# Kernel optimization log

Measured on AMD Instinct MI355X. Metric: run time of the kernel, lower is better.

The kernel has to match this reference:

```python
import math
import jax, jax.numpy as jnp
import numpy as np

B, S, T = 32, 512, 180
D, F, L, H = 512, 2048, 6, 8
DH = D // H


def _pos_encoding(length, d):
    pos = np.arange(length, dtype=np.float32)[:, None]
    div = np.exp(np.arange(0, d, 2, dtype=np.float32) * (-math.log(10000.0) / d))
    pe = np.zeros((length, d), dtype=np.float32)
    pe[:, 0::2] = np.sin(pos * div)
    pe[:, 1::2] = np.cos(pos * div)
    return jnp.asarray(pe)


def _ln(x, scale, bias):
    mu = x.mean(-1, keepdims=True)
    var = ((x - mu) ** 2).mean(-1, keepdims=True)
    return (x - mu) * jax.lax.rsqrt(var + 1e-5) * scale + bias


def _mha(q_in, kv_in, w, b, causal=False):
    # w: [4, D, D] = (Wq, Wk, Wv, Wo); b: [4, D]
    b_, sq = q_in.shape[:2]
    q = (q_in @ w[0] + b[0]).reshape(b_, sq, H, DH)
    k = (kv_in @ w[1] + b[1]).reshape(b_, -1, H, DH)
    v = (kv_in @ w[2] + b[2]).reshape(b_, -1, H, DH)
    s = jnp.einsum('bqhd,bkhd->bhqk', q, k) / math.sqrt(DH)
    if causal:
        mask = jnp.tril(jnp.ones((sq, k.shape[1]), dtype=bool))
        s = jnp.where(mask, s, -1e9)
    a = jax.nn.softmax(s, axis=-1)
    o = jnp.einsum('bhqk,bkhd->bqhd', a, v).reshape(b_, sq, D)
    return o @ w[3] + b[3]


def _ffn(x, w1, b1, w2, b2):
    return jax.nn.relu(x @ w1 + b1) @ w2 + b2


def setup_inputs() -> dict:
    key = jax.random.key(0)
    ks = jax.random.split(key, 16)
    n = lambda k, shape: jax.random.normal(k, shape, jnp.float32) * 0.02
    return {
        'x': jax.random.normal(ks[0], (B, S, 2), jnp.float32),
        'y_cv_teacher': jax.random.normal(ks[1], (B, T, 1), jnp.float32),
        'src_proj_w': n(ks[2], (2, D)), 'src_proj_b': jnp.zeros((D,), jnp.float32),
        'tgt_proj_w': n(ks[3], (1, D)), 'tgt_proj_b': jnp.zeros((D,), jnp.float32),
        'enc_attn_w': n(ks[4], (L, 4, D, D)), 'enc_attn_b': jnp.zeros((L, 4, D), jnp.float32),
        'enc_ffn_w1': n(ks[5], (L, D, F)), 'enc_ffn_b1': jnp.zeros((L, F), jnp.float32),
        'enc_ffn_w2': n(ks[6], (L, F, D)), 'enc_ffn_b2': jnp.zeros((L, D), jnp.float32),
        'enc_ln_scale': jnp.ones((L, 2, D), jnp.float32), 'enc_ln_bias': jnp.zeros((L, 2, D), jnp.float32),
        'dec_self_w': n(ks[7], (L, 4, D, D)), 'dec_self_b': jnp.zeros((L, 4, D), jnp.float32),
        'dec_cross_w': n(ks[8], (L, 4, D, D)), 'dec_cross_b': jnp.zeros((L, 4, D), jnp.float32),
        'dec_ffn_w1': n(ks[9], (L, D, F)), 'dec_ffn_b1': jnp.zeros((L, F), jnp.float32),
        'dec_ffn_w2': n(ks[10], (L, F, D)), 'dec_ffn_b2': jnp.zeros((L, D), jnp.float32),
        'dec_ln_scale': jnp.ones((L, 3, D), jnp.float32), 'dec_ln_bias': jnp.zeros((L, 3, D), jnp.float32),
        'out_w': n(ks[11], (D, 1)), 'out_b': jnp.zeros((1,), jnp.float32),
    }


def reference(x, y_cv_teacher, src_proj_w, src_proj_b, tgt_proj_w, tgt_proj_b,
              enc_attn_w, enc_attn_b, enc_ffn_w1, enc_ffn_b1, enc_ffn_w2, enc_ffn_b2,
              enc_ln_scale, enc_ln_bias, dec_self_w, dec_self_b, dec_cross_w, dec_cross_b,
              dec_ffn_w1, dec_ffn_b1, dec_ffn_w2, dec_ffn_b2, dec_ln_scale, dec_ln_bias,
              out_w, out_b):
    pe = _pos_encoding(512, D)
    # encoder (post-norm, relu FFN, dropout disabled = eval semantics)
    h = x @ src_proj_w + src_proj_b + pe[: x.shape[1]]
    for i in range(L):
        h = _ln(h + _mha(h, h, enc_attn_w[i], enc_attn_b[i]), enc_ln_scale[i, 0], enc_ln_bias[i, 0])
        h = _ln(h + _ffn(h, enc_ffn_w1[i], enc_ffn_b1[i], enc_ffn_w2[i], enc_ffn_b2[i]),
                enc_ln_scale[i, 1], enc_ln_bias[i, 1])
    memory = h
    # teacher-forced decoder input: [start=0, y_cv_teacher[:-1]]
    tgt_in = jnp.concatenate([jnp.zeros((x.shape[0], 1, 1), x.dtype), y_cv_teacher[:, :-1, :]], axis=1)
    d = tgt_in @ tgt_proj_w + tgt_proj_b + pe[: tgt_in.shape[1]]
    for i in range(L):
        d = _ln(d + _mha(d, d, dec_self_w[i], dec_self_b[i], causal=True),
                dec_ln_scale[i, 0], dec_ln_bias[i, 0])
        d = _ln(d + _mha(d, memory, dec_cross_w[i], dec_cross_b[i]),
                dec_ln_scale[i, 1], dec_ln_bias[i, 1])
        d = _ln(d + _ffn(d, dec_ffn_w1[i], dec_ffn_b1[i], dec_ffn_w2[i], dec_ffn_b2[i]),
                dec_ln_scale[i, 2], dec_ln_bias[i, 2])
    return d @ out_w + out_b  # [B, T, 1]
```

## Files before the change

### kernel.cpp

```cpp
#include <hip/hip_runtime.h>
#include <math.h>

#define B_  32
#define S_  512
#define T_  180
#define D_  512
#define F_  2048
#define L_  6
#define H_  8
#define DH_ 64

typedef unsigned short u16;
typedef __attribute__((ext_vector_type(8))) short short8;
typedef __attribute__((ext_vector_type(4))) float floatx4;

__device__ __forceinline__ float bf2f(u16 h) {
    union { unsigned u; float f; } un; un.u = ((unsigned)h) << 16; return un.f;
}
__device__ __forceinline__ u16 f2bf(float f) {
    union { float f; unsigned u; } un; un.f = f;
    unsigned u = un.u;
    u += 0x7fffu + ((u >> 16) & 1u);
    return (u16)(u >> 16);
}

__device__ __forceinline__ void gload16(const u16* g, u16* l) {
    __builtin_amdgcn_global_load_lds(
        (const __attribute__((address_space(1))) void*)g,
        (__attribute__((address_space(3))) void*)l, 16, 0, 0);
}

__device__ __forceinline__ float pos_enc(int pos, int c) {
    int i2 = c & ~1;
    float div = expf(-(float)i2 * (9.210340371976184f / 512.0f));
    float arg = (float)pos * div;
    return (c & 1) ? cosf(arg) : sinf(arg);
}

__global__ __launch_bounds__(256) void embed_src_kernel(
    const float* __restrict__ x, const float* __restrict__ w,
    const float* __restrict__ b, u16* __restrict__ h)
{
    int idx = blockIdx.x * 256 + threadIdx.x;
    if (idx >= B_ * S_ * D_) return;
    int c  = idx & (D_ - 1);
    int bs = idx >> 9;
    int s  = bs & (S_ - 1);
    float x0 = x[bs * 2 + 0];
    float x1 = x[bs * 2 + 1];
    h[idx] = f2bf(x0 * w[c] + x1 * w[D_ + c] + b[c] + pos_enc(s, c));
}

__global__ __launch_bounds__(256) void embed_tgt_kernel(
    const float* __restrict__ y, const float* __restrict__ w,
    const float* __restrict__ b, u16* __restrict__ d)
{
    int idx = blockIdx.x * 256 + threadIdx.x;
    if (idx >= B_ * T_ * D_) return;
    int c  = idx & (D_ - 1);
    int bt = idx >> 9;
    int t  = bt % T_;
    int bb = bt / T_;
    float tv = (t == 0) ? 0.0f : y[bb * T_ + (t - 1)];
    d[idx] = f2bf(tv * w[c] + b[c] + pos_enc(t, c));
}

__global__ __launch_bounds__(256) void wconv_kernel(
    const float* __restrict__ W, u16* __restrict__ Wt, int K, int N)
{
    __shared__ float tile[32][33];
    size_t mat = (size_t)blockIdx.z * K * N;
    const float* Wm = W + mat;
    u16* Wtm = Wt + mat;
    int n0 = blockIdx.x * 32, k0 = blockIdx.y * 32;
    int tx = threadIdx.x & 31, ty = threadIdx.x >> 5;
#pragma unroll
    for (int i = 0; i < 32; i += 8)
        tile[ty + i][tx] = Wm[(size_t)(k0 + ty + i) * N + n0 + tx];
    __syncthreads();
#pragma unroll
    for (int i = 0; i < 32; i += 8)
        Wtm[(size_t)(n0 + ty + i) * K + k0 + tx] = f2bf(tile[tx][ty + i]);
}

__global__ __launch_bounds__(256) void gemm_bf16_kernel(
    const u16* __restrict__ A, int lda, const u16* __restrict__ Bt,
    const float* __restrict__ bias, u16* __restrict__ C, int ldc,
    int M, int N, int K, int relu)
{
    __shared__ u16 smem[18432];
    u16* As = smem;
    u16* Bs = smem + 8192;

    int tid  = threadIdx.x;
    int w    = tid >> 6;
    int lane = tid & 63;
    int m0 = blockIdx.y << 7, n0 = blockIdx.x << 7;

    int sr = w * 32 + (lane >> 2);
    int sk = (lane & 3) * 8;
    const u16* ag0 = A  + (size_t)(m0 + sr)      * lda + sk;
    const u16* ag1 = A  + (size_t)(m0 + sr + 16) * lda + sk;
    const u16* bg0 = Bt + (size_t)(n0 + sr)      * K + sk;
    const u16* bg1 = Bt + (size_t)(n0 + sr + 16) * K + sk;
    u16* al0 = As + (w * 2 + 0) * 512;
    u16* al1 = As + (w * 2 + 1) * 512;
    u16* bl0 = Bs + (w * 2 + 0) * 512;
    u16* bl1 = Bs + (w * 2 + 1) * 512;

    int wm = (w >> 1) * 64, wn = (w & 1) * 64;
    int fr = lane & 15;
    int fk = (lane >> 4) * 8;

    floatx4 acc[4][4] = {};

    for (int k0 = 0; k0 < K; k0 += 64) {
#pragma unroll
        for (int hh = 0; hh < 2; ++hh) {
            int go = k0 + hh * 32;
            int lo = hh * 4096;
            gload16(ag0 + go, al0 + lo);
            gload16(ag1 + go, al1 + lo);
            gload16(bg0 + go, bl0 + lo);
            gload16(bg1 + go, bl1 + lo);
        }
        __syncthreads();

#pragma unroll
        for (int hh = 0; hh < 2; ++hh) {
            int lo = hh * 4096;
            short8 af[4], bf[4];
#pragma unroll
            for (int i = 0; i < 4; ++i)
                af[i] = *(const short8*)&As[lo + (wm + i * 16 + fr) * 32 + fk];
#pragma unroll
            for (int j = 0; j < 4; ++j)
                bf[j] = *(const short8*)&Bs[lo + (wn + j * 16 + fr) * 32 + fk];
#pragma unroll
            for (int i = 0; i < 4; ++i)
#pragma unroll
                for (int j = 0; j < 4; ++j)
                    acc[i][j] = __builtin_amdgcn_mfma_f32_16x16x32_bf16(
                        af[i], bf[j], acc[i][j], 0, 0, 0);
        }
        __syncthreads();
    }

    u16* epi = smem + w * 4608;
    int cc = lane & 15;
    int rq = (lane >> 4) * 4;
#pragma unroll
    for (int j = 0; j < 4; ++j) {
        float bj = bias[n0 + wn + j * 16 + cc];
#pragma unroll
        for (int i = 0; i < 4; ++i) {
#pragma unroll
            for (int r = 0; r < 4; ++r) {
                float vv = acc[i][j][r] + bj;
                if (relu) vv = fmaxf(vv, 0.f);
                epi[(i * 16 + rq + r) * 72 + j * 16 + cc] = f2bf(vv);
            }
        }
    }
    __syncthreads();
#pragma unroll
    for (int t = 0; t < 8; ++t) {
        int er = t * 8 + (lane >> 3);
        int ec = (lane & 7) * 8;
        short8 vv = *(const short8*)&epi[er * 72 + ec];
        *(short8*)&C[(size_t)(m0 + wm + er) * ldc + n0 + wn + ec] = vv;
    }
}

#define CEXP 0.1803368801111244f

__global__ __launch_bounds__(256) void attn_mfma_kernel(
    const u16* Q, int qs, const u16* __restrict__ K, int ks,
    const u16* __restrict__ V, u16* O,
    int Sq, int Sk, int causal)
{
    __shared__ u16 Qs[64 * 72];
    __shared__ u16 Ks[64 * 72];
    __shared__ u16 Vt[64 * 72];
    __shared__ u16 Ps[4][16 * 72];

    int tid  = threadIdx.x;
    int w    = tid >> 6;
    int lane = tid & 63;
    int n    = lane & 15;
    int quad = lane >> 4;
    int bh = blockIdx.x;
    int bb = bh >> 3, hhd = bh & 7;
    int q0 = blockIdx.y * 64;

    const u16* Qb = Q + (size_t)bb * Sq * qs + hhd * DH_;
    const u16* Kb = K + (size_t)bb * Sk * ks + hhd * DH_;
    const u16* Vb = V + (size_t)bb * Sk * ks + hhd * DH_;

#pragma unroll
    for (int it = 0; it < 2; ++it) {
        int idx = it * 256 + tid;
        int r = idx >> 3, dg = (idx & 7) * 8;
        int qg = q0 + r;
        short8 vv = {};
        if (qg < Sq) vv = *(const short8*)&Qb[(size_t)qg * qs + dg];
        *(short8*)&Qs[r * 72 + dg] = vv;
    }

    float m_i[4], l_i[4];
    floatx4 o_acc[4] = {};
#pragma unroll
    for (int r = 0; r < 4; ++r) { m_i[r] = -1e30f; l_i[r] = 0.f; }

    int qrow0 = q0 + w * 16 + quad * 4;
    int kend = causal ? ((Sk < q0 + 64) ? Sk : (q0 + 64)) : Sk;
    __syncthreads();

    for (int k0 = 0; k0 < kend; k0 += 64) {
#pragma unroll
        for (int it = 0; it < 2; ++it) {
            int idx = it * 256 + tid;
            int r = idx >> 3, dg = (idx & 7) * 8;
            int kg = k0 + r;
            short8 kv = {}, vv = {};
            if (kg < Sk) {
                kv = *(const short8*)&Kb[(size_t)kg * ks + dg];
                vv = *(const short8*)&Vb[(size_t)kg * ks + dg];
            }
            *(short8*)&Ks[r * 72 + dg] = kv;
            int col = (r + dg) & 63;
#pragma unroll
            for (int j = 0; j < 8; ++j)
                Vt[(dg + j) * 72 + col] = (u16)vv[j];
        }
        __syncthreads();

        floatx4 sc[4] = {};
        short8 aq0 = *(const short8*)&Qs[(w * 16 + n) * 72 + quad * 8];
        short8 aq1 = *(const short8*)&Qs[(w * 16 + n) * 72 + 32 + quad * 8];
#pragma unroll
        for (int j = 0; j < 4; ++j) {
            short8 bk0 = *(const short8*)&Ks[(j * 16 + n) * 72 + quad * 8];
            short8 bk1 = *(const short8*)&Ks[(j * 16 + n) * 72 + 32 + quad * 8];
            sc[j] = __builtin_amdgcn_mfma_f32_16x16x32_bf16(aq0, bk0, sc[j], 0, 0, 0);
            sc[j] = __builtin_amdgcn_mfma_f32_16x16x32_bf16(aq1, bk1, sc[j], 0, 0, 0);
        }

        bool need_mask = (k0 + 64 > Sk) ||
                         (causal && (k0 + 63 > q0 + w * 16));
        if (need_mask) {
#pragma unroll
            for (int j = 0; j < 4; ++j) {
                int kg = k0 + j * 16 + n;
#pragma unroll
                for (int r = 0; r < 4; ++r) {
                    if (kg >= Sk || (causal && kg > qrow0 + r))
                        sc[j][r] = -1e30f;
                }
            }
        }

#pragma unroll
        for (int r = 0; r < 4; ++r) {
            float mx = fmaxf(fmaxf(sc[0][r], sc[1][r]), fmaxf(sc[2][r], sc[3][r]));
#pragma unroll
            for (int off = 8; off > 0; off >>= 1)
                mx = fmaxf(mx, __shfl_xor(mx, off, 16));
            float mnew = fmaxf(m_i[r], mx);
            float alpha = exp2f((m_i[r] - mnew) * CEXP);
            m_i[r] = mnew;
            float ps = 0.f;
#pragma unroll
            for (int j = 0; j < 4; ++j) {
                float p = exp2f((sc[j][r] - mnew) * CEXP);
                sc[j][r] = p; ps += p;
            }
#pragma unroll
            for (int off = 8; off > 0; off >>= 1)
                ps += __shfl_xor(ps, off, 16);
            l_i[r] = l_i[r] * alpha + ps;
#pragma unroll
            for (int jb = 0; jb < 4; ++jb) o_acc[jb][r] *= alpha;
        }

#pragma unroll
        for (int j = 0; j < 4; ++j)
#pragma unroll
            for (int r = 0; r < 4; ++r)
                Ps[w][(quad * 4 + r) * 72 + j * 16 + n] = f2bf(sc[j][r]);

        short8 ap0 = *(const short8*)&Ps[w][n * 72 + quad * 8];
        short8 ap1 = *(const short8*)&Ps[w][n * 72 + 32 + quad * 8];
#pragma unroll
        for (int jb = 0; jb < 4; ++jb) {
            int d = jb * 16 + n;
            int rot = d & ~7;
            short8 bv0 = *(const short8*)&Vt[d * 72 + ((quad * 8 + rot) & 63)];
            short8 bv1 = *(const short8*)&Vt[d * 72 + ((32 + quad * 8 + rot) & 63)];
            o_acc[jb] = __builtin_amdgcn_mfma_f32_16x16x32_bf16(ap0, bv0, o_acc[jb], 0, 0, 0);
            o_acc[jb] = __builtin_amdgcn_mfma_f32_16x16x32_bf16(ap1, bv1, o_acc[jb], 0, 0, 0);
        }
        __syncthreads();
    }

    float inv[4];
#pragma unroll
    for (int r = 0; r < 4; ++r) inv[r] = 1.0f / l_i[r];
    u16* Ob = O + (size_t)bb * Sq * qs + hhd * DH_;
#pragma unroll
    for (int r = 0; r < 4; ++r) {
        int qg = qrow0 + r;
        if (qg < Sq) {
#pragma unroll
            for (int jb = 0; jb < 4; ++jb)
                Ob[(size_t)qg * qs + jb * 16 + n] = f2bf(o_acc[jb][r] * inv[r]);
        }
    }
}

__global__ __launch_bounds__(128) void add_ln_kernel(
    u16* __restrict__ h, const u16* __restrict__ delta,
    const float* __restrict__ scale, const float* __restrict__ bias)
{
    __shared__ float red[2][2];
    int row = blockIdx.x, tid = threadIdx.x;
    int lane = tid & 63, wv = tid >> 6;
    size_t base = (size_t)row * D_ + tid * 4;
    uint2 hv = *(const uint2*)&h[base];
    uint2 dv = *(const uint2*)&delta[base];
    float v0 = bf2f(hv.x & 0xffff) + bf2f(dv.x & 0xffff);
    float v1 = bf2f(hv.x >> 16)    + bf2f(dv.x >> 16);
    float v2 = bf2f(hv.y & 0xffff) + bf2f(dv.y & 0xffff);
    float v3 = bf2f(hv.y >> 16)    + bf2f(dv.y >> 16);

    float a  = v0 + v1 + v2 + v3;
    float b2 = v0 * v0 + v1 * v1 + v2 * v2 + v3 * v3;
#pragma unroll
    for (int off = 32; off > 0; off >>= 1) {
        a  += __shfl_xor(a, off);
        b2 += __shfl_xor(b2, off);
    }
    if (lane == 0) { red[wv][0] = a; red[wv][1] = b2; }
    __syncthreads();
    float S1 = red[0][0] + red[1][0];
    float S2 = red[0][1] + red[1][1];
    float mu = S1 * (1.0f / 512.0f);
    float var = S2 * (1.0f / 512.0f) - mu * mu;
    float rs = rsqrtf(var + 1e-5f);

    int c = tid * 4;
    float4 sc = *(const float4*)&scale[c];
    float4 bi = *(const float4*)&bias[c];
    unsigned lo = (unsigned)f2bf((v0 - mu) * rs * sc.x + bi.x) |
                  ((unsigned)f2bf((v1 - mu) * rs * sc.y + bi.y) << 16);
    unsigned hi = (unsigned)f2bf((v2 - mu) * rs * sc.z + bi.z) |
                  ((unsigned)f2bf((v3 - mu) * rs * sc.w + bi.w) << 16);
    *(uint2*)&h[base] = make_uint2(lo, hi);
}

__global__ __launch_bounds__(64) void out_proj_kernel(
    const u16* __restrict__ d, const float* __restrict__ w,
    const float* __restrict__ b, float* __restrict__ out)
{
    int row = blockIdx.x, lane = threadIdx.x;
    float s = 0.f;
    for (int c = lane; c < D_; c += 64) s += bf2f(d[(size_t)row * D_ + c]) * w[c];
#pragma unroll
    for (int off = 32; off > 0; off >>= 1) s += __shfl_down(s, off);
    if (lane == 0) out[row] = s + b[0];
}

extern "C" void kernel_launch(void* const* d_in, const int* in_sizes, int n_in,
                              void* d_out, int out_size, void* d_ws, size_t ws_size,
                              hipStream_t stream)
{
    const float* x          = (const float*)d_in[0];
    const float* y          = (const float*)d_in[1];
    const float* src_w      = (const float*)d_in[2];
    const float* src_b      = (const float*)d_in[3];
    const float* tgt_w      = (const float*)d_in[4];
    const float* tgt_b      = (const float*)d_in[5];
    const float* enc_attn_w = (const float*)d_in[6];
    const float* enc_attn_b = (const float*)d_in[7];
    const float* enc_ffn_w1 = (const float*)d_in[8];
    const float* enc_ffn_b1 = (const float*)d_in[9];
    const float* enc_ffn_w2 = (const float*)d_in[10];
    const float* enc_ffn_b2 = (const float*)d_in[11];
    const float* enc_ln_s   = (const float*)d_in[12];
    const float* enc_ln_b   = (const float*)d_in[13];
    const float* dec_self_w = (const float*)d_in[14];
    const float* dec_self_b = (const float*)d_in[15];
    const float* dec_cross_w= (const float*)d_in[16];
    const float* dec_cross_b= (const float*)d_in[17];
    const float* dec_ffn_w1 = (const float*)d_in[18];
    const float* dec_ffn_b1 = (const float*)d_in[19];
    const float* dec_ffn_w2 = (const float*)d_in[20];
    const float* dec_ffn_b2 = (const float*)d_in[21];
    const float* dec_ln_s   = (const float*)d_in[22];
    const float* dec_ln_b   = (const float*)d_in[23];
    const float* out_w      = (const float*)d_in[24];
    const float* out_b      = (const float*)d_in[25];
    float* out = (float*)d_out;

    const size_t E_BSD = (size_t)B_ * S_ * D_;
    const size_t E_BTD = (size_t)B_ * T_ * D_;
    const size_t WDD   = (size_t)D_ * D_;
    const size_t WDF   = (size_t)D_ * F_;
    const int MS = B_ * S_;
    const int MT = B_ * T_;

    u16* h    = (u16*)d_ws;
    u16* qkv  = h + E_BSD;
    u16* o    = qkv + (size_t)MS * 1536;
    u16* dbuf = o + E_BSD;
    u16* wsc  = dbuf + E_BTD;
    u16* mid  = qkv;
    u16* cq   = qkv;
    u16* ckv  = qkv + 4 * 1024 * 1024;

    auto gemm = [&](const u16* A, int lda, const u16* Wt, const float* bi,
                    u16* C, int ldc, int M, int N, int K, int relu) {
        dim3 g(N / 128, M / 128);
        gemm_bf16_kernel<<<g, dim3(256), 0, stream>>>(A, lda, Wt, bi, C, ldc,
                                                      M, N, K, relu);
    };
    auto attn = [&](const u16* Qp, int qs, const u16* Kp, int ks,
                    const u16* Vp, u16* Op, int Sq, int Sk, int causal) {
        dim3 g(B_ * H_, (Sq + 63) / 64);
        attn_mfma_kernel<<<g, dim3(256), 0, stream>>>(Qp, qs, Kp, ks, Vp, Op,
                                                      Sq, Sk, causal);
    };
    auto addln = [&](u16* hp, const u16* dp, const float* sc, const float* bi,
                     int rows) {
        add_ln_kernel<<<dim3(rows), dim3(128), 0, stream>>>(hp, dp, sc, bi);
    };
    auto wconv = [&](const float* W, u16* Wt, int K, int N, int nmat) {
        wconv_kernel<<<dim3(N / 32, K / 32, nmat), dim3(256), 0, stream>>>(W, Wt, K, N);
    };

    embed_src_kernel<<<dim3((B_ * S_ * D_ + 255) / 256), dim3(256), 0, stream>>>(
        x, src_w, src_b, h);
    for (int l = 0; l < L_; ++l) {
        wconv(enc_attn_w + (size_t)l * 4 * WDD, wsc, D_, D_, 4);
        wconv(enc_ffn_w1 + (size_t)l * WDF, wsc + 4 * WDD, D_, F_, 1);
        wconv(enc_ffn_w2 + (size_t)l * WDF, wsc + 4 * WDD + WDF, F_, D_, 1);

        const float* bl = enc_attn_b + (size_t)l * 4 * D_;
        gemm(h, D_, wsc, bl, qkv, 1536, MS, 1536, D_, 0);
        attn(qkv, 1536, qkv + 512, 1536, qkv + 1024, qkv, S_, S_, 0);
        gemm(qkv, 1536, wsc + 3 * WDD, bl + 3 * D_, o, D_, MS, D_, D_, 0);
        addln(h, o, enc_ln_s + (size_t)l * 2 * D_, enc_ln_b + (size_t)l * 2 * D_, MS);

        for (int m0 = 0; m0 < MS; m0 += 8192) {
            gemm(h + (size_t)m0 * D_, D_, wsc + 4 * WDD,
                 enc_ffn_b1 + (size_t)l * F_, mid, F_, 8192, F_, D_, 1);
            gemm(mid, F_, wsc + 4 * WDD + WDF, enc_ffn_b2 + (size_t)l * D_,
                 o + (size_t)m0 * D_, D_, 8192, D_, F_, 0);
        }
        addln(h, o, enc_ln_s + (size_t)l * 2 * D_ + D_,
              enc_ln_b + (size_t)l * 2 * D_ + D_, MS);
    }

    embed_tgt_kernel<<<dim3((B_ * T_ * D_ + 255) / 256), dim3(256), 0, stream>>>(
        y, tgt_w, tgt_b, dbuf);
    for (int l = 0; l < L_; ++l) {
        wconv(dec_self_w  + (size_t)l * 4 * WDD, wsc, D_, D_, 4);
        wconv(dec_cross_w + (size_t)l * 4 * WDD, wsc + 4 * WDD, D_, D_, 4);
        wconv(dec_ffn_w1  + (size_t)l * WDF, wsc + 8 * WDD, D_, F_, 1);
        wconv(dec_ffn_w2  + (size_t)l * WDF, wsc + 8 * WDD + WDF, F_, D_, 1);

        const float* bl = dec_self_b + (size_t)l * 4 * D_;
        gemm(dbuf, D_, wsc, bl, qkv, 1536, MT, 1536, D_, 0);
        attn(qkv, 1536, qkv + 512, 1536, qkv + 1024, qkv, T_, T_, 1);
        gemm(qkv, 1536, wsc + 3 * WDD, bl + 3 * D_, o, D_, MT, D_, D_, 0);
        addln(dbuf, o, dec_ln_s + (size_t)l * 3 * D_,
              dec_ln_b + (size_t)l * 3 * D_, MT);

        const float* bc = dec_cross_b + (size_t)l * 4 * D_;
        gemm(h, D_, wsc + 5 * WDD, bc + D_, ckv, 1024, MS, 1024, D_, 0);
        gemm(dbuf, D_, wsc + 4 * WDD, bc, cq, D_, MT, D_, D_, 0);
        attn(cq, 512, ckv, 1024, ckv + 512, cq, T_, S_, 0);
        gemm(cq, D_, wsc + 7 * WDD, bc + 3 * D_, o, D_, MT, D_, D_, 0);
        addln(dbuf, o, dec_ln_s + (size_t)l * 3 * D_ + D_,
              dec_ln_b + (size_t)l * 3 * D_ + D_, MT);

        gemm(dbuf, D_, wsc + 8 * WDD, dec_ffn_b1 + (size_t)l * F_,
             mid, F_, MT, F_, D_, 1);
        gemm(mid, F_, wsc + 8 * WDD + WDF, dec_ffn_b2 + (size_t)l * D_,
             o, D_, MT, D_, F_, 0);
        addln(dbuf, o, dec_ln_s + (size_t)l * 3 * D_ + 2 * D_,
              dec_ln_b + (size_t)l * 3 * D_ + 2 * D_, MT);
    }

    out_proj_kernel<<<dim3(MT), dim3(64), 0, stream>>>(dbuf, out_w, out_b, out);
}
```

Before: 3.495 ms.

## Emit V projection transposed and use swizzled V tiles in attention

Adds a GEMM variant that writes the V projection directly in a per-batch transposed [D, S] layout, and a new attention kernel that loads V rows contiguously into an XOR-swizzled shared tile. The aim is to avoid the in-kernel V transpose and its strided shared-memory writes in the encoder self-attention and decoder cross-attention. The QKV projection is split into a QK GEMM plus a separate transposed-V GEMM, which means an extra launch and a less efficient scattered epilogue. Decoder self-attention keeps the old path. The causal flag is dropped from the new kernel, which is fine because both callers are non-causal.

```diff
diff --git a/kernel.cpp b/kernel.cpp
--- a/kernel.cpp
+++ b/kernel.cpp
@@ -172,7 +172,218 @@
     }
 }
 
+__global__ __launch_bounds__(256) void gemm_bf16_t_kernel(
+    const u16* __restrict__ A, int lda, const u16* __restrict__ Bt,
+    const float* __restrict__ bias, u16* __restrict__ Ct,
+    int M, int N, int K)
+{
+    __shared__ u16 smem[17408];
+    u16* As = smem;
+    u16* Bs = smem + 8192;
+
+    int tid  = threadIdx.x;
+    int w    = tid >> 6;
+    int lane = tid & 63;
+    int m0 = blockIdx.y << 7, n0 = blockIdx.x << 7;
+
+    int sr = w * 32 + (lane >> 2);
+    int sk = (lane & 3) * 8;
+    const u16* ag0 = A  + (size_t)(m0 + sr)      * lda + sk;
+    const u16* ag1 = A  + (size_t)(m0 + sr + 16) * lda + sk;
+    const u16* bg0 = Bt + (size_t)(n0 + sr)      * K + sk;
+    const u16* bg1 = Bt + (size_t)(n0 + sr + 16) * K + sk;
+    u16* al0 = As + (w * 2 + 0) * 512;
+    u16* al1 = As + (w * 2 + 1) * 512;
+    u16* bl0 = Bs + (w * 2 + 0) * 512;
+    u16* bl1 = Bs + (w * 2 + 1) * 512;
+
+    int wm = (w >> 1) * 64, wn = (w & 1) * 64;
+    int fr = lane & 15;
+    int fk = (lane >> 4) * 8;
+
+    floatx4 acc[4][4] = {};
+
+    for (int k0 = 0; k0 < K; k0 += 64) {
+#pragma unroll
+        for (int hh = 0; hh < 2; ++hh) {
+            int go = k0 + hh * 32;
+            int lo = hh * 4096;
+            gload16(ag0 + go, al0 + lo);
+            gload16(ag1 + go, al1 + lo);
+            gload16(bg0 + go, bl0 + lo);
+            gload16(bg1 + go, bl1 + lo);
+        }
+        __syncthreads();
+
+#pragma unroll
+        for (int hh = 0; hh < 2; ++hh) {
+            int lo = hh * 4096;
+            short8 af[4], bf[4];
+#pragma unroll
+            for (int i = 0; i < 4; ++i)
+                af[i] = *(const short8*)&As[lo + (wm + i * 16 + fr) * 32 + fk];
+#pragma unroll
+            for (int j = 0; j < 4; ++j)
+                bf[j] = *(const short8*)&Bs[lo + (wn + j * 16 + fr) * 32 + fk];
+#pragma unroll
+            for (int i = 0; i < 4; ++i)
+#pragma unroll
+                for (int j = 0; j < 4; ++j)
+                    acc[i][j] = __builtin_amdgcn_mfma_f32_16x16x32_bf16(
+                        af[i], bf[j], acc[i][j], 0, 0, 0);
+        }
+        __syncthreads();
+    }
+
+    u16* epi = smem;
+    int cc = lane & 15;
+    int rq = (lane >> 4) * 4;
+#pragma unroll
+    for (int j = 0; j < 4; ++j) {
+        float bj = bias[n0 + wn + j * 16 + cc];
+#pragma unroll
+        for (int i = 0; i < 4; ++i) {
+            unsigned lo = (unsigned)f2bf(acc[i][j][0] + bj) |
+                          ((unsigned)f2bf(acc[i][j][1] + bj) << 16);
+            unsigned hi = (unsigned)f2bf(acc[i][j][2] + bj) |
+                          ((unsigned)f2bf(acc[i][j][3] + bj) << 16);
+            *(uint2*)&epi[(size_t)(wn + j * 16 + cc) * 136 + wm + i * 16 + rq] =
+                make_uint2(lo, hi);
+        }
+    }
+    __syncthreads();
+    int bb2 = m0 >> 9;
+    int s0  = m0 & 511;
+#pragma unroll
+    for (int tt = 0; tt < 8; ++tt) {
+        int dloc = tt * 16 + (tid >> 4);
+        int sloc = (tid & 15) * 8;
+        short8 vv = *(const short8*)&epi[dloc * 136 + sloc];
+        *(short8*)&Ct[(size_t)bb2 * N * 512 + (size_t)(n0 + dloc) * 512 + s0 + sloc] = vv;
+    }
+}
+
 #define CEXP 0.1803368801111244f
+
+__global__ __launch_bounds__(256) void attn2_kernel(
+    const u16* Q, int qs, const u16* __restrict__ K, int ks,
+    const u16* __restrict__ Vt, u16* O, int Sq, int Sk)
+{
+    __shared__ u16 Qs[64 * 72];
+    __shared__ u16 Ks[64 * 72];
+    __shared__ u16 Vs[64 * 64];
+    __shared__ u16 Ps[4][16 * 72];
+
+    int tid  = threadIdx.x;
+    int w    = tid >> 6;
+    int lane = tid & 63;
+    int n    = lane & 15;
+    int quad = lane >> 4;
+    int bh = blockIdx.x;
+    int bb = bh >> 3, hhd = bh & 7;
+    int q0 = blockIdx.y * 64;
+
+    const u16* Qb = Q  + (size_t)bb * Sq * qs + hhd * DH_;
+    const u16* Kb = K  + (size_t)bb * Sk * ks + hhd * DH_;
+    const u16* Vb = Vt + ((size_t)bb * D_ + hhd * DH_) * Sk;
+
+#pragma unroll
+    for (int it = 0; it < 2; ++it) {
+        int idx = it * 256 + tid;
+        int r = idx >> 3, dg = (idx & 7) * 8;
+        int qg = q0 + r;
+        short8 vv = {};
+        if (qg < Sq) vv = *(const short8*)&Qb[(size_t)qg * qs + dg];
+        *(short8*)&Qs[r * 72 + dg] = vv;
+    }
+
+    float m_i[4], l_i[4];
+    floatx4 o_acc[4] = {};
+#pragma unroll
+    for (int r = 0; r < 4; ++r) { m_i[r] = -1e30f; l_i[r] = 0.f; }
+    __syncthreads();
+
+    for (int k0 = 0; k0 < Sk; k0 += 64) {
+#pragma unroll
+        for (int it = 0; it < 2; ++it) {
+            int idx = it * 256 + tid;
+            int r = idx >> 3, dg = (idx & 7) * 8;
+            short8 kv = *(const short8*)&Kb[(size_t)(k0 + r) * ks + dg];
+            *(short8*)&Ks[r * 72 + dg] = kv;
+            short8 vv = *(const short8*)&Vb[(size_t)r * Sk + k0 + (idx & 7) * 8];
+            *(short8*)&Vs[r * 64 + (((idx & 7) ^ (r & 7)) * 8)] = vv;
+        }
+        __syncthreads();
+
+        floatx4 sc[4] = {};
+        short8 aq0 = *(const short8*)&Qs[(w * 16 + n) * 72 + quad * 8];
+        short8 aq1 = *(const short8*)&Qs[(w * 16 + n) * 72 + 32 + quad * 8];
+#pragma unroll
+        for (int j = 0; j < 4; ++j) {
+            short8 bk0 = *(const short8*)&Ks[(j * 16 + n) * 72 + quad * 8];
+            short8 bk1 = *(const short8*)&Ks[(j * 16 + n) * 72 + 32 + quad * 8];
+            sc[j] = __builtin_amdgcn_mfma_f32_16x16x32_bf16(aq0, bk0, sc[j], 0, 0, 0);
+            sc[j] = __builtin_amdgcn_mfma_f32_16x16x32_bf16(aq1, bk1, sc[j], 0, 0, 0);
+        }
+
+#pragma unroll
+        for (int r = 0; r < 4; ++r) {
+            float mx = fmaxf(fmaxf(sc[0][r], sc[1][r]), fmaxf(sc[2][r], sc[3][r]));
+#pragma unroll
+            for (int off = 8; off > 0; off >>= 1)
+                mx = fmaxf(mx, __shfl_xor(mx, off, 16));
+            float mnew = fmaxf(m_i[r], mx);
+            float alpha = exp2f((m_i[r] - mnew) * CEXP);
+            m_i[r] = mnew;
+            float ps = 0.f;
+#pragma unroll
+            for (int j = 0; j < 4; ++j) {
+                float p = exp2f((sc[j][r] - mnew) * CEXP);
+                sc[j][r] = p; ps += p;
+            }
+#pragma unroll
+            for (int off = 8; off > 0; off >>= 1)
+                ps += __shfl_xor(ps, off, 16);
+            l_i[r] = l_i[r] * alpha + ps;
+#pragma unroll
+            for (int jb = 0; jb < 4; ++jb) o_acc[jb][r] *= alpha;
+        }
+
+#pragma unroll
+        for (int j = 0; j < 4; ++j)
+#pragma unroll
+            for (int r = 0; r < 4; ++r)
+                Ps[w][(quad * 4 + r) * 72 + j * 16 + n] = f2bf(sc[j][r]);
+
+        short8 ap0 = *(const short8*)&Ps[w][n * 72 + quad * 8];
+        short8 ap1 = *(const short8*)&Ps[w][n * 72 + 32 + quad * 8];
+#pragma unroll
+        for (int jb = 0; jb < 4; ++jb) {
+            int d = jb * 16 + n;
+            int sw = d & 7;
+            short8 bv0 = *(const short8*)&Vs[d * 64 + ((quad ^ sw) * 8)];
+            short8 bv1 = *(const short8*)&Vs[d * 64 + (((quad + 4) ^ sw) * 8)];
+            o_acc[jb] = __builtin_amdgcn_mfma_f32_16x16x32_bf16(ap0, bv0, o_acc[jb], 0, 0, 0);
+            o_acc[jb] = __builtin_amdgcn_mfma_f32_16x16x32_bf16(ap1, bv1, o_acc[jb], 0, 0, 0);
+        }
+        __syncthreads();
+    }
+
+    int qrow0 = q0 + w * 16 + quad * 4;
+    float inv[4];
+#pragma unroll
+    for (int r = 0; r < 4; ++r) inv[r] = 1.0f / l_i[r];
+    u16* Ob = O + (size_t)bb * Sq * qs + hhd * DH_;
+#pragma unroll
+    for (int r = 0; r < 4; ++r) {
+        int qg = qrow0 + r;
+        if (qg < Sq) {
+#pragma unroll
+            for (int jb = 0; jb < 4; ++jb)
+                Ob[(size_t)qg * qs + jb * 16 + n] = f2bf(o_acc[jb][r] * inv[r]);
+        }
+    }
+}
 
 __global__ __launch_bounds__(256) void attn_mfma_kernel(
     const u16* Q, int qs, const u16* __restrict__ K, int ks,
@@ -410,13 +621,14 @@
     const int MT = B_ * T_;
 
     u16* h    = (u16*)d_ws;
-    u16* qkv  = h + E_BSD;
-    u16* o    = qkv + (size_t)MS * 1536;
+    u16* qk   = h + E_BSD;
+    u16* o    = qk + (size_t)MS * 1024;
     u16* dbuf = o + E_BSD;
     u16* wsc  = dbuf + E_BTD;
-    u16* mid  = qkv;
-    u16* cq   = qkv;
-    u16* ckv  = qkv + 4 * 1024 * 1024;
+    u16* vt   = wsc + 8 * WDD + 2 * WDF;
+    u16* mid  = qk;
+    u16* ck   = qk;
+    u16* cq   = qk + E_BSD;
 
     auto gemm = [&](const u16* A, int lda, const u16* Wt, const float* bi,
                     u16* C, int ldc, int M, int N, int K, int relu) {
@@ -424,8 +636,18 @@
         gemm_bf16_kernel<<<g, dim3(256), 0, stream>>>(A, lda, Wt, bi, C, ldc,
                                                       M, N, K, relu);
     };
-    auto attn = [&](const u16* Qp, int qs, const u16* Kp, int ks,
-                    const u16* Vp, u16* Op, int Sq, int Sk, int causal) {
+    auto gemm_t = [&](const u16* A, int lda, const u16* Wt, const float* bi,
+                      u16* Ct, int M, int N, int K) {
+        dim3 g(N / 128, M / 128);
+        gemm_bf16_t_kernel<<<g, dim3(256), 0, stream>>>(A, lda, Wt, bi, Ct, M, N, K);
+    };
+    auto attn2 = [&](const u16* Qp, int qs, const u16* Kp, int ks,
+                     const u16* Vtp, u16* Op, int Sq, int Sk) {
+        dim3 g(B_ * H_, (Sq + 63) / 64);
+        attn2_kernel<<<g, dim3(256), 0, stream>>>(Qp, qs, Kp, ks, Vtp, Op, Sq, Sk);
+    };
+    auto attn_old = [&](const u16* Qp, int qs, const u16* Kp, int ks,
+                        const u16* Vp, u16* Op, int Sq, int Sk, int causal) {
         dim3 g(B_ * H_, (Sq + 63) / 64);
         attn_mfma_kernel<<<g, dim3(256), 0, stream>>>(Qp, qs, Kp, ks, Vp, Op,
                                                       Sq, Sk, causal);
@@ -446,9 +668,10 @@
         wconv(enc_ffn_w2 + (size_t)l * WDF, wsc + 4 * WDD + WDF, F_, D_, 1);
 
         const float* bl = enc_attn_b + (size_t)l * 4 * D_;
-        gemm(h, D_, wsc, bl, qkv, 1536, MS, 1536, D_, 0);
-        attn(qkv, 1536, qkv + 512, 1536, qkv + 1024, qkv, S_, S_, 0);
-        gemm(qkv, 1536, wsc + 3 * WDD, bl + 3 * D_, o, D_, MS, D_, D_, 0);
+        gemm(h, D_, wsc, bl, qk, 1024, MS, 1024, D_, 0);
+        gemm_t(h, D_, wsc + 2 * WDD, bl + 2 * D_, vt, MS, D_, D_);
+        attn2(qk, 1024, qk + 512, 1024, vt, qk, S_, S_);
+        gemm(qk, 1024, wsc + 3 * WDD, bl + 3 * D_, o, D_, MS, D_, D_, 0);
         addln(h, o, enc_ln_s + (size_t)l * 2 * D_, enc_ln_b + (size_t)l * 2 * D_, MS);
 
         for (int m0 = 0; m0 < MS; m0 += 8192) {
@@ -470,16 +693,17 @@
         wconv(dec_ffn_w2  + (size_t)l * WDF, wsc + 8 * WDD + WDF, F_, D_, 1);
 
         const float* bl = dec_self_b + (size_t)l * 4 * D_;
-        gemm(dbuf, D_, wsc, bl, qkv, 1536, MT, 1536, D_, 0);
-        attn(qkv, 1536, qkv + 512, 1536, qkv + 1024, qkv, T_, T_, 1);
-        gemm(qkv, 1536, wsc + 3 * WDD, bl + 3 * D_, o, D_, MT, D_, D_, 0);
+        gemm(dbuf, D_, wsc, bl, qk, 1536, MT, 1536, D_, 0);
+        attn_old(qk, 1536, qk + 512, 1536, qk + 1024, qk, T_, T_, 1);
+        gemm(qk, 1536, wsc + 3 * WDD, bl + 3 * D_, o, D_, MT, D_, D_, 0);
         addln(dbuf, o, dec_ln_s + (size_t)l * 3 * D_,
               dec_ln_b + (size_t)l * 3 * D_, MT);
 
         const float* bc = dec_cross_b + (size_t)l * 4 * D_;
-        gemm(h, D_, wsc + 5 * WDD, bc + D_, ckv, 1024, MS, 1024, D_, 0);
+        gemm(h, D_, wsc + 5 * WDD, bc + D_, ck, 512, MS, D_, D_, 0);
+        gemm_t(h, D_, wsc + 6 * WDD, bc + 2 * D_, vt, MS, D_, D_);
         gemm(dbuf, D_, wsc + 4 * WDD, bc, cq, D_, MT, D_, D_, 0);
-        attn(cq, 512, ckv, 1024, ckv + 512, cq, T_, S_, 0);
+        attn2(cq, 512, ck, 512, vt, cq, T_, S_);
         gemm(cq, D_, wsc + 7 * WDD, bc + 3 * D_, o, D_, MT, D_, D_, 0);
         addln(dbuf, o, dec_ln_s + (size_t)l * 3 * D_ + D_,
               dec_ln_b + (size_t)l * 3 * D_ + D_, MT);
```

Result: no change. 3.540 ms (+1.3%).
